# Kernel tuning notes

Measured on AMD Instinct MI355X. Metric: run time of the kernel, lower is better.

## Reference

```python
import jax, jax.numpy as jnp
import numpy as np

N, D, E = 16384, 1024, 8

def setup_inputs() -> dict:
    key = jax.random.key(0)
    ks = jax.random.split(key, 5)
    s = 1.0 / np.sqrt(D)
    return {
        "x": jax.random.normal(ks[0], (N, D), dtype=jnp.float32),
        "router_w": jax.random.uniform(ks[1], (E, D), jnp.float32, -s, s),   # torch Linear weight [out,in]
        "router_b": jax.random.uniform(ks[2], (E,), jnp.float32, -s, s),
        "expert_w": jax.random.uniform(ks[3], (E, D, D), jnp.float32, -s, s),  # [E, out, in]
        "expert_b": jax.random.uniform(ks[4], (E, D), jnp.float32, -s, s),
    }

def reference(x, router_w, router_b, expert_w, expert_b):
    # Router: logits -> softmax -> argmax (argmax of softmax == argmax of logits)
    logits = x @ router_w.T + router_b            # [N, E]
    top = jnp.argmax(logits, axis=-1)             # [N]
    # Compute all expert outputs (vectorized grouped GEMM), then select top-1.
    # Faithful to the torch loop: output is the raw expert output, NOT gate-scaled.
    xe = jnp.einsum('nd,eod->neo', x, expert_w) + expert_b[None, :, :]  # [N, E, D]
    out = jnp.take_along_axis(xe, top[:, None, None], axis=1)[:, 0, :]  # [N, D]
    return out
```

## Files before the change

### kernel.cpp

```cpp
#include <hip/hip_runtime.h>
#include <hip/hip_bf16.h>


#define NTOK 16384
#define DIM  1024
#define NEXP 8

#define AS1 __attribute__((address_space(1)))
#define AS3 __attribute__((address_space(3)))

typedef __bf16 bf16x8 __attribute__((ext_vector_type(8)));
typedef float  f32x4  __attribute__((ext_vector_type(4)));

__device__ __forceinline__ unsigned int f2bf(float f) {
  unsigned int u = __builtin_bit_cast(unsigned int, f);
  u += 0x7FFFu + ((u >> 16) & 1u);
  return u >> 16;
}

__global__ __launch_bounds__(256) void k_router(const float* __restrict__ x,
                                                const float* __restrict__ rw,
                                                const float* __restrict__ rb,
                                                unsigned short* __restrict__ xbf,
                                                int* __restrict__ top) {
  __shared__ float wlds[NEXP * DIM];
  const int tid = threadIdx.x;
  const int lane = tid & 63;
  const int wave = tid >> 6;
#pragma unroll
  for (int i = 0; i < 8; ++i)
    ((float4*)wlds)[tid + 256 * i] = ((const float4*)rw)[tid + 256 * i];
  __syncthreads();

  const int ea = lane & 7;
  const float bias = rb[ea];

#pragma unroll 1
  for (int tp = 0; tp < 2; ++tp) {
    const int nA = (blockIdx.x << 4) + (wave << 2) + (tp << 1);
    const int nB = nA + 1;

    float4 xa[4], xb[4];
#pragma unroll
    for (int j = 0; j < 4; ++j) {
      xa[j] = *(const float4*)(x + ((size_t)nA << 10) + (j << 8) + (lane << 2));
      xb[j] = *(const float4*)(x + ((size_t)nB << 10) + (j << 8) + (lane << 2));
    }

#pragma unroll
    for (int j = 0; j < 4; ++j) {
      uint2 sa, sb;
      sa.x = f2bf(xa[j].x) | (f2bf(xa[j].y) << 16);
      sa.y = f2bf(xa[j].z) | (f2bf(xa[j].w) << 16);
      sb.x = f2bf(xb[j].x) | (f2bf(xb[j].y) << 16);
      sb.y = f2bf(xb[j].z) | (f2bf(xb[j].w) << 16);
      *(uint2*)(xbf + ((size_t)nA << 10) + (j << 8) + (lane << 2)) = sa;
      *(uint2*)(xbf + ((size_t)nB << 10) + (j << 8) + (lane << 2)) = sb;
    }

    double pA[8] = {}, pB[8] = {};
#pragma unroll
    for (int j = 0; j < 4; ++j) {
#pragma unroll
      for (int e = 0; e < 8; ++e) {
        float4 wv = *(const float4*)&wlds[e * 1024 + (j << 8) + (lane << 2)];
        pA[e] += (double)xa[j].x * (double)wv.x;
        pA[e] += (double)xa[j].y * (double)wv.y;
        pA[e] += (double)xa[j].z * (double)wv.z;
        pA[e] += (double)xa[j].w * (double)wv.w;
        pB[e] += (double)xb[j].x * (double)wv.x;
        pB[e] += (double)xb[j].y * (double)wv.y;
        pB[e] += (double)xb[j].z * (double)wv.z;
        pB[e] += (double)xb[j].w * (double)wv.w;
      }
      __builtin_amdgcn_sched_barrier(0);
    }

    float qA[8], qB[8];
#pragma unroll
    for (int e = 0; e < 8; ++e) { qA[e] = (float)pA[e]; qB[e] = (float)pB[e]; }
#pragma unroll
    for (int e = 0; e < 8; ++e) {
      qA[e] += __shfl_xor(qA[e], 1);
      qB[e] += __shfl_xor(qB[e], 1);
      qA[e] += __shfl_xor(qA[e], 2);
      qB[e] += __shfl_xor(qB[e], 2);
      qA[e] += __shfl_xor(qA[e], 4);
      qB[e] += __shfl_xor(qB[e], 4);
    }
    float sA, sB;
    {
      float q0 = (ea & 1) ? qA[1] : qA[0], q1 = (ea & 1) ? qA[3] : qA[2];
      float q2 = (ea & 1) ? qA[5] : qA[4], q3 = (ea & 1) ? qA[7] : qA[6];
      float r0 = (ea & 2) ? q1 : q0, r1 = (ea & 2) ? q3 : q2;
      sA = (ea & 4) ? r1 : r0;
      q0 = (ea & 1) ? qB[1] : qB[0]; q1 = (ea & 1) ? qB[3] : qB[2];
      q2 = (ea & 1) ? qB[5] : qB[4]; q3 = (ea & 1) ? qB[7] : qB[6];
      r0 = (ea & 2) ? q1 : q0; r1 = (ea & 2) ? q3 : q2;
      sB = (ea & 4) ? r1 : r0;
    }
    sA += __shfl_xor(sA, 8);  sB += __shfl_xor(sB, 8);
    sA += __shfl_xor(sA, 16); sB += __shfl_xor(sB, 16);
    sA += __shfl_xor(sA, 32); sB += __shfl_xor(sB, 32);
    sA += bias; sB += bias;
    float bvA = sA, bvB = sB;
    int biA = ea, biB = ea;
#pragma unroll
    for (int mask = 1; mask <= 4; mask <<= 1) {
      float ovA = __shfl_xor(bvA, mask), ovB = __shfl_xor(bvB, mask);
      int oiA = __shfl_xor(biA, mask), oiB = __shfl_xor(biB, mask);
      if (ovA > bvA || (ovA == bvA && oiA < biA)) { bvA = ovA; biA = oiA; }
      if (ovB > bvB || (ovB == bvB && oiB < biB)) { bvB = ovB; biB = oiB; }
    }
    if (lane == 0) {
      top[nA] = biA;
      top[nB] = biB;
    }
  }
}

__global__ __launch_bounds__(1024) void k_sortconv(const float* __restrict__ ew,
                                                   unsigned short* __restrict__ wbf,
                                                   const int* __restrict__ top,
                                                   int* __restrict__ counts,
                                                   int* __restrict__ tok) {
  const int t = threadIdx.x;
  if (blockIdx.x > 0) {
    size_t i = ((size_t)(blockIdx.x - 1) * 1024 + t) * 8;
    const float4* p = (const float4*)(ew + i);
    float4 a = p[0], b = p[1];
    unsigned int w0 = f2bf(a.x) | (f2bf(a.y) << 16);
    unsigned int w1 = f2bf(a.z) | (f2bf(a.w) << 16);
    unsigned int w2 = f2bf(b.x) | (f2bf(b.y) << 16);
    unsigned int w3 = f2bf(b.z) | (f2bf(b.w) << 16);
    *(uint4*)(wbf + i) = make_uint4(w0, w1, w2, w3);
    return;
  }

  __shared__ unsigned long long sc[2][2][1024];
  int4 v[4];
  const int4* tp = (const int4*)(top + t * 16);
#pragma unroll
  for (int i = 0; i < 4; ++i) v[i] = tp[i];

  unsigned long long h0 = 0, h1 = 0;
#pragma unroll
  for (int i = 0; i < 16; ++i) {
    int e = ((const int*)v)[i];
    if (e < 4) h0 += 1ull << (16 * e);
    else       h1 += 1ull << (16 * (e - 4));
  }
  sc[0][0][t] = h0;
  sc[0][1][t] = h1;
  __syncthreads();

  int cur = 0;
  for (int s = 1; s < 1024; s <<= 1) {
    unsigned long long a0 = sc[cur][0][t], a1 = sc[cur][1][t];
    if (t >= s) { a0 += sc[cur][0][t - s]; a1 += sc[cur][1][t - s]; }
    sc[cur ^ 1][0][t] = a0;
    sc[cur ^ 1][1][t] = a1;
    cur ^= 1;
    __syncthreads();
  }

  unsigned long long b0 = sc[cur][0][t] - h0;
  unsigned long long b1 = sc[cur][1][t] - h1;
  if (t == 1023) {
    unsigned long long i0 = sc[cur][0][t], i1 = sc[cur][1][t];
#pragma unroll
    for (int e = 0; e < 4; ++e) counts[e] = (int)((i0 >> (16 * e)) & 0xFFFF);
#pragma unroll
    for (int e = 0; e < 4; ++e) counts[4 + e] = (int)((i1 >> (16 * e)) & 0xFFFF);
  }
#pragma unroll
  for (int i = 0; i < 16; ++i) {
    int e = ((const int*)v)[i];
    int pos;
    if (e < 4) {
      pos = (int)((b0 >> (16 * e)) & 0xFFFF);
      b0 += 1ull << (16 * e);
    } else {
      int f = e - 4;
      pos = (int)((b1 >> (16 * f)) & 0xFFFF);
      b1 += 1ull << (16 * f);
    }
    tok[(e << 14) + pos] = t * 16 + i;
  }
}

__global__ __launch_bounds__(256, 2) void k_gemm(const unsigned short* __restrict__ xbf,
                                                 const unsigned short* __restrict__ wbf,
                                                 const float* __restrict__ eb,
                                                 const int* __restrict__ counts,
                                                 const int* __restrict__ tokall,
                                                 float* __restrict__ out) {
  const int bid = blockIdx.x;
  const int e = bid & 7;
  const int loc = bid >> 3;
  const int cb = loc & 7;
  const int t = loc >> 3;
  const int c = counts[e];
  if (t * 128 >= c) return;
  const int n0 = cb << 7;
  const int* tok = tokall + (e << 14);
  const int tid = threadIdx.x;
  const int lane = tid & 63;
  const int wave = tid >> 6;

  __shared__ unsigned short As[2][128 * 64];
  __shared__ unsigned short Bs[2][128 * 64];

  const int prow = tid >> 3;
  const int pchk = tid & 7;
  size_t asrc[4], bsrc[4];
  const unsigned short* wb = wbf + ((size_t)e << 20);
#pragma unroll
  for (int s = 0; s < 4; ++s) {
    int row = s * 32 + prow;
    int m = t * 128 + row;
    int g = tok[(m < c) ? m : 0];
    int l = pchk ^ (row & 7);
    asrc[s] = (size_t)g * DIM + (size_t)l * 8;
    bsrc[s] = (size_t)(n0 + row) * DIM + (size_t)l * 8;
  }

  f32x4 acc[4][4] = {};
  const int wr = wave >> 1, wc = wave & 1;

  int aoff[2][4], boff[2][4];
#pragma unroll
  for (int h = 0; h < 2; ++h)
#pragma unroll
    for (int m = 0; m < 4; ++m) {
      int row = wr * 64 + m * 16 + (lane & 15);
      int p = (h * 4 + (lane >> 4)) ^ (row & 7);
      aoff[h][m] = row * 64 + p * 8;
      int rowb = wc * 64 + m * 16 + (lane & 15);
      int pb = (h * 4 + (lane >> 4)) ^ (rowb & 7);
      boff[h][m] = rowb * 64 + pb * 8;
    }

  auto stage = [&](int b, int k0) {
#pragma unroll
    for (int s = 0; s < 4; ++s) {
      __builtin_amdgcn_global_load_lds(
          (const AS1 unsigned int*)(xbf + asrc[s] + k0),
          (AS3 unsigned int*)(&As[b][s * 2048 + wave * 512]),
          16, 0, 0);
      __builtin_amdgcn_global_load_lds(
          (const AS1 unsigned int*)(wb + bsrc[s] + k0),
          (AS3 unsigned int*)(&Bs[b][s * 2048 + wave * 512]),
          16, 0, 0);
    }
  };

  stage(0, 0);
  for (int k = 0; k < 16; ++k) {
    if (k < 15) {
      stage((k + 1) & 1, (k + 1) * 64);
      asm volatile("s_waitcnt vmcnt(8)" ::: "memory");
    } else {
      asm volatile("s_waitcnt vmcnt(0)" ::: "memory");
    }
    __builtin_amdgcn_s_barrier();
    __builtin_amdgcn_sched_barrier(0);
    const unsigned short* Ab = As[k & 1];
    const unsigned short* Bb = Bs[k & 1];
#pragma unroll
    for (int h = 0; h < 2; ++h) {
      bf16x8 af[4], bfr[4];
#pragma unroll
      for (int m = 0; m < 4; ++m) af[m] = *(const bf16x8*)&Ab[aoff[h][m]];
#pragma unroll
      for (int n = 0; n < 4; ++n) bfr[n] = *(const bf16x8*)&Bb[boff[h][n]];
#pragma unroll
      for (int m = 0; m < 4; ++m)
#pragma unroll
        for (int n = 0; n < 4; ++n)
          acc[m][n] = __builtin_amdgcn_mfma_f32_16x16x32_bf16(af[m], bfr[n], acc[m][n], 0, 0, 0);
    }
    __builtin_amdgcn_s_barrier();
  }

  const int colb = n0 + wc * 64 + (lane & 15);
  float bias[4];
#pragma unroll
  for (int n = 0; n < 4; ++n) bias[n] = eb[(e << 10) + colb + n * 16];
#pragma unroll
  for (int m = 0; m < 4; ++m) {
    int rbase = t * 128 + wr * 64 + m * 16 + ((lane >> 4) << 2);
#pragma unroll
    for (int r = 0; r < 4; ++r) {
      int mm = rbase + r;
      if (mm < c) {
        int g = tok[mm];
        float* op = out + ((size_t)g << 10);
#pragma unroll
        for (int n = 0; n < 4; ++n) op[colb + n * 16] = acc[m][n][r] + bias[n];
      }
    }
  }
}

extern "C" void kernel_launch(void* const* d_in, const int* in_sizes, int n_in,
                              void* d_out, int out_size, void* d_ws, size_t ws_size,
                              hipStream_t stream) {
  const float* x  = (const float*)d_in[0];
  const float* rw = (const float*)d_in[1];
  const float* rb = (const float*)d_in[2];
  const float* ew = (const float*)d_in[3];
  const float* eb = (const float*)d_in[4];
  float* out = (float*)d_out;

  char* ws = (char*)d_ws;
  unsigned short* wbf = (unsigned short*)ws;
  unsigned short* xbf = (unsigned short*)(ws + (16u << 20));
  int* tok    = (int*)(ws + (48u << 20));
  int* counts = (int*)(ws + (48u << 20) + (1u << 19));
  int* top    = (int*)(ws + (48u << 20) + (1u << 19) + 128);

  k_router<<<NTOK / 16, 256, 0, stream>>>(x, rw, rb, xbf, top);
  k_sortconv<<<1025, 1024, 0, stream>>>(ew, wbf, top, counts, tok);
  k_gemm<<<8192, 256, 0, stream>>>(xbf, wbf, eb, counts, tok, out);
}
```

Before: 100.8 us.

## Move expert weight conversion into router kernel and use wave-shuffle prefix scan

Expert weight fp32-to-bf16 conversion now runs in the odd blocks of the router kernel, so it overlaps with routing instead of sitting in the single-block sort kernel, which is serialized after the router. The sort kernel becomes a one-block kernel that uses wave-level shuffle scans plus a small cross-wave combine instead of a 10-step LDS Hillis-Steele scan with barriers. The cost is that the odd conversion blocks still allocate the router's 32KB of shared memory, which can limit occupancy.

```diff
diff --git a/kernel.cpp b/kernel.cpp
--- a/kernel.cpp
+++ b/kernel.cpp
@@ -21,10 +21,30 @@
 __global__ __launch_bounds__(256) void k_router(const float* __restrict__ x,
                                                 const float* __restrict__ rw,
                                                 const float* __restrict__ rb,
+                                                const float* __restrict__ ew,
                                                 unsigned short* __restrict__ xbf,
+                                                unsigned short* __restrict__ wbf,
                                                 int* __restrict__ top) {
   __shared__ float wlds[NEXP * DIM];
   const int tid = threadIdx.x;
+
+  if (blockIdx.x & 1) {
+    const int cb = blockIdx.x >> 1;
+#pragma unroll
+    for (int pass = 0; pass < 4; ++pass) {
+      size_t i = ((size_t)(pass * 1024 + cb) * 256 + tid) * 8;
+      const float4* p = (const float4*)(ew + i);
+      float4 a = p[0], b = p[1];
+      unsigned int w0 = f2bf(a.x) | (f2bf(a.y) << 16);
+      unsigned int w1 = f2bf(a.z) | (f2bf(a.w) << 16);
+      unsigned int w2 = f2bf(b.x) | (f2bf(b.y) << 16);
+      unsigned int w3 = f2bf(b.z) | (f2bf(b.w) << 16);
+      *(uint4*)(wbf + i) = make_uint4(w0, w1, w2, w3);
+    }
+    return;
+  }
+
+  const int rbid = blockIdx.x >> 1;
   const int lane = tid & 63;
   const int wave = tid >> 6;
 #pragma unroll
@@ -37,7 +57,7 @@
 
 #pragma unroll 1
   for (int tp = 0; tp < 2; ++tp) {
-    const int nA = (blockIdx.x << 4) + (wave << 2) + (tp << 1);
+    const int nA = (rbid << 4) + (wave << 2) + (tp << 1);
     const int nB = nA + 1;
 
     float4 xa[4], xb[4];
@@ -119,25 +139,14 @@
   }
 }
 
-__global__ __launch_bounds__(1024) void k_sortconv(const float* __restrict__ ew,
-                                                   unsigned short* __restrict__ wbf,
-                                                   const int* __restrict__ top,
-                                                   int* __restrict__ counts,
-                                                   int* __restrict__ tok) {
+__global__ __launch_bounds__(1024) void k_sort(const int* __restrict__ top,
+                                               int* __restrict__ counts,
+                                               int* __restrict__ tok) {
+  __shared__ unsigned long long wsum[2][16];
   const int t = threadIdx.x;
-  if (blockIdx.x > 0) {
-    size_t i = ((size_t)(blockIdx.x - 1) * 1024 + t) * 8;
-    const float4* p = (const float4*)(ew + i);
-    float4 a = p[0], b = p[1];
-    unsigned int w0 = f2bf(a.x) | (f2bf(a.y) << 16);
-    unsigned int w1 = f2bf(a.z) | (f2bf(a.w) << 16);
-    unsigned int w2 = f2bf(b.x) | (f2bf(b.y) << 16);
-    unsigned int w3 = f2bf(b.z) | (f2bf(b.w) << 16);
-    *(uint4*)(wbf + i) = make_uint4(w0, w1, w2, w3);
-    return;
-  }
-
-  __shared__ unsigned long long sc[2][2][1024];
+  const int lane = t & 63;
+  const int wv = t >> 6;
+
   int4 v[4];
   const int4* tp = (const int4*)(top + t * 16);
 #pragma unroll
@@ -150,29 +159,33 @@
     if (e < 4) h0 += 1ull << (16 * e);
     else       h1 += 1ull << (16 * (e - 4));
   }
-  sc[0][0][t] = h0;
-  sc[0][1][t] = h1;
+
+  unsigned long long s0 = h0, s1 = h1;
+#pragma unroll
+  for (int d = 1; d < 64; d <<= 1) {
+    unsigned long long t0 = __shfl_up(s0, d);
+    unsigned long long t1 = __shfl_up(s1, d);
+    if (lane >= d) { s0 += t0; s1 += t1; }
+  }
+  if (lane == 63) { wsum[0][wv] = s0; wsum[1][wv] = s1; }
   __syncthreads();
 
-  int cur = 0;
-  for (int s = 1; s < 1024; s <<= 1) {
-    unsigned long long a0 = sc[cur][0][t], a1 = sc[cur][1][t];
-    if (t >= s) { a0 += sc[cur][0][t - s]; a1 += sc[cur][1][t - s]; }
-    sc[cur ^ 1][0][t] = a0;
-    sc[cur ^ 1][1][t] = a1;
-    cur ^= 1;
-    __syncthreads();
-  }
-
-  unsigned long long b0 = sc[cur][0][t] - h0;
-  unsigned long long b1 = sc[cur][1][t] - h1;
+  unsigned long long base0 = 0, base1 = 0;
+#pragma unroll
+  for (int i = 0; i < 15; ++i) {
+    if (i < wv) { base0 += wsum[0][i]; base1 += wsum[1][i]; }
+  }
+  unsigned long long b0 = base0 + s0 - h0;
+  unsigned long long b1 = base1 + s1 - h1;
+
   if (t == 1023) {
-    unsigned long long i0 = sc[cur][0][t], i1 = sc[cur][1][t];
+    unsigned long long i0 = base0 + s0, i1 = base1 + s1;
 #pragma unroll
     for (int e = 0; e < 4; ++e) counts[e] = (int)((i0 >> (16 * e)) & 0xFFFF);
 #pragma unroll
     for (int e = 0; e < 4; ++e) counts[4 + e] = (int)((i1 >> (16 * e)) & 0xFFFF);
   }
+
 #pragma unroll
   for (int i = 0; i < 16; ++i) {
     int e = ((const int*)v)[i];
@@ -320,7 +333,7 @@
   int* counts = (int*)(ws + (48u << 20) + (1u << 19));
   int* top    = (int*)(ws + (48u << 20) + (1u << 19) + 128);
 
-  k_router<<<NTOK / 16, 256, 0, stream>>>(x, rw, rb, xbf, top);
-  k_sortconv<<<1025, 1024, 0, stream>>>(ew, wbf, top, counts, tok);
+  k_router<<<2048, 256, 0, stream>>>(x, rw, rb, ew, xbf, wbf, top);
+  k_sort<<<1, 1024, 0, stream>>>(top, counts, tok);
   k_gemm<<<8192, 256, 0, stream>>>(xbf, wbf, eb, counts, tok, out);
 }
```

Result: slower. 108.0 us (+7.2%).
